# Optimization experiments

Measured on AMD Instinct MI355X. Metric: run time of the kernel, lower is better.

## Reference

```python
import jax, jax.numpy as jnp
import numpy as np

S, B, E, H, M = 1024, 4, 1024, 16, 128  # seq, batch, embed, heads, model_dims (key width)
V = E // H                              # value_dims = 64
_WSCALE = 1.0 / np.sqrt(E)              # keep softmax logits O(1)


def _cplx(re, im):
    return jax.lax.complex(re, im)


def setup_inputs() -> dict:
    key = jax.random.key(0)
    ks = jax.random.split(key, 10)
    n = lambda k, shp: jax.random.normal(k, shp, dtype=jnp.float32)
    w = lambda k, shp: n(k, shp) * np.float32(_WSCALE / np.sqrt(2.0))
    return {
        "logits_re": n(ks[0], (S, B, E)),
        "logits_im": n(ks[1], (S, B, E)),
        "wq_re": w(ks[2], (H, M, E)), "wq_im": w(ks[3], (H, M, E)),
        "wk_re": w(ks[4], (H, M, E)), "wk_im": w(ks[5], (H, M, E)),
        "wv_re": w(ks[6], (H, V, E)), "wv_im": w(ks[7], (H, V, E)),
        "wo_re": w(ks[8], (E, E)),    "wo_im": w(ks[9], (E, E)),
    }


def reference(logits_re, logits_im, wq_re, wq_im, wk_re, wk_im,
              wv_re, wv_im, wo_re, wo_im):
    x = _cplx(logits_re, logits_im)          # (s, b, e) complex64
    wq = _cplx(wq_re, wq_im)                 # (h, m, e)
    wk = _cplx(wk_re, wk_im)
    wv = _cplx(wv_re, wv_im)                 # (h, v, e)
    wo = _cplx(wo_re, wo_im)                 # (e, e)

    q = jnp.einsum('hme,sbe->bhsm', wq, x)   # (b, h, s, m)
    k = jnp.einsum('hme,sbe->bhsm', wk, x)
    v = jnp.einsum('hve,sbe->bhsv', wv, x)   # (b, h, s, v)

    scores = jnp.einsum('bhsm,bhtm->bhst', q, k)         # complex, no conjugation (matches torch matmul)
    amp = jnp.abs(scores)                                # -> float32
    causal = jnp.triu(jnp.ones((S, S), dtype=bool), 1)   # True above diagonal -> masked
    amp = jnp.where(causal, -jnp.inf, amp) / jnp.sqrt(jnp.float32(M))
    attn = jax.nn.softmax(amp, axis=-1).astype(scores.dtype)  # cast back to complex64

    upd = jnp.einsum('bhst,bhtv->bhsv', attn, v)         # (b, h, s, v)
    upd = upd.transpose(2, 0, 1, 3).reshape(S, B, E)     # 's2 b (h v)'
    out = jnp.einsum('sbe,ef->sbf', upd, wo) + x         # residual
    # complex output returned as stacked (real, imag) float32 for harness compatibility
    return jnp.stack([out.real, out.imag])
```

## Files before the change

### kernel.cpp

```cpp
#include <hip/hip_runtime.h>
#include <math.h>

#define S_DIM 1024
#define B_DIM 4
#define E_DIM 1024
#define H_DIM 16
#define M_DIM 128
#define V_DIM 64

typedef __attribute__((ext_vector_type(8))) short short8;
typedef __attribute__((ext_vector_type(4))) float f32x4;
typedef __attribute__((ext_vector_type(4))) int int4v;

__device__ __forceinline__ unsigned short f2bf(float f) {
    union { float f; unsigned u; } v; v.f = f;
    unsigned r = v.u + 0x7FFFu + ((v.u >> 16) & 1u);
    return (unsigned short)(r >> 16);
}

__device__ __forceinline__ void async16(const unsigned short* g, unsigned short* l) {
    __builtin_amdgcn_global_load_lds(
        (const __attribute__((address_space(1))) void*)g,
        (__attribute__((address_space(3))) void*)l,
        16, 0, 0);
}

__global__ __launch_bounds__(256) void convert_all(
    const float* __restrict__ xre,  const float* __restrict__ xim,
    const float* __restrict__ wqre, const float* __restrict__ wqim,
    const float* __restrict__ wkre, const float* __restrict__ wkim,
    const float* __restrict__ wvre, const float* __restrict__ wvim,
    unsigned short* __restrict__ xbre, unsigned short* __restrict__ xbim,
    unsigned short* __restrict__ wbre, unsigned short* __restrict__ wbim)
{
    const int i = blockIdx.x * 256 + threadIdx.x;
    const float *re, *im;
    unsigned short *dr, *di;
    int j;
    if (i < 1048576)      { re = xre;  im = xim;  dr = xbre;               di = xbim;               j = i; }
    else if (i < 1572864) { re = wqre; im = wqim; dr = wbre;               di = wbim;               j = i - 1048576; }
    else if (i < 2097152) { re = wkre; im = wkim; dr = wbre + 2048 * 1024; di = wbim + 2048 * 1024; j = i - 1572864; }
    else                  { re = wvre; im = wvim; dr = wbre + 4096 * 1024; di = wbim + 4096 * 1024; j = i - 2097152; }
    float4 r = ((const float4*)re)[j];
    float4 m = ((const float4*)im)[j];
    ushort4 ro, mo;
    ro.x = f2bf(r.x); ro.y = f2bf(r.y); ro.z = f2bf(r.z); ro.w = f2bf(r.w);
    mo.x = f2bf(m.x); mo.y = f2bf(m.y); mo.z = f2bf(m.z); mo.w = f2bf(m.w);
    ((ushort4*)dr)[j] = ro;
    ((ushort4*)di)[j] = mo;
}

__global__ __launch_bounds__(256) void transpose_wo(
    const float* __restrict__ wore, const float* __restrict__ woim,
    unsigned short* __restrict__ wtre, unsigned short* __restrict__ wtim)
{
    __shared__ float tr[32][33], ti[32][33];
    const int bx = blockIdx.x * 32;
    const int by = blockIdx.y * 32;
    const int tx = threadIdx.x & 31, ty = threadIdx.x >> 5;
    for (int i = ty; i < 32; i += 8) {
        tr[i][tx] = wore[(bx + i) * E_DIM + by + tx];
        ti[i][tx] = woim[(bx + i) * E_DIM + by + tx];
    }
    __syncthreads();
    for (int i = ty; i < 32; i += 8) {
        wtre[(by + i) * E_DIM + bx + tx] = f2bf(tr[tx][i]);
        wtim[(by + i) * E_DIM + bx + tx] = f2bf(ti[tx][i]);
    }
}

__global__ __launch_bounds__(256) void vtrans(
    const unsigned short* __restrict__ vrp, const unsigned short* __restrict__ vip,
    unsigned short* __restrict__ vrt, unsigned short* __restrict__ vit)
{
    __shared__ unsigned short tl[2][64][66];
    const int tid = threadIdx.x;
    const int t0 = blockIdx.x * 64;
    const int bh = blockIdx.y;
    #pragma unroll
    for (int pl = 0; pl < 2; ++pl) {
        const unsigned short* src = pl ? vip : vrp;
        #pragma unroll
        for (int p = 0; p < 2; ++p) {
            const int row = p * 32 + (tid >> 3);
            const int col = (tid & 7) * 8;
            short8 d = *(const short8*)&src[((size_t)bh * S_DIM + t0 + row) * V_DIM + col];
            #pragma unroll
            for (int j = 0; j < 8; ++j) tl[pl][row][col + j] = (unsigned short)d[j];
        }
    }
    __syncthreads();
    #pragma unroll
    for (int pl = 0; pl < 2; ++pl) {
        unsigned short* dst = pl ? vit : vrt;
        #pragma unroll
        for (int p = 0; p < 2; ++p) {
            const int v = p * 32 + (tid >> 3);
            const int tc = (tid & 7) * 8;
            short8 d;
            #pragma unroll
            for (int j = 0; j < 8; ++j) d[j] = (short)tl[pl][tc + j][v];
            *(short8*)&dst[((size_t)bh * V_DIM + v) * S_DIM + t0 + tc] = d;
        }
    }
}

template<int MODE>
__global__ __launch_bounds__(256, 2) void cgemm(
    const unsigned short* __restrict__ Are, const unsigned short* __restrict__ Aim,
    const unsigned short* __restrict__ Bre, const unsigned short* __restrict__ Bim,
    unsigned short* __restrict__ qrp, unsigned short* __restrict__ qip,
    unsigned short* __restrict__ krp, unsigned short* __restrict__ kip,
    unsigned short* __restrict__ vrp, unsigned short* __restrict__ vip,
    const float* __restrict__ xre, const float* __restrict__ xim,
    float* __restrict__ out)
{
    __shared__ __align__(16) unsigned short lds[32768];
    const int tid  = threadIdx.x;
    const int wave = tid >> 6;
    const int lane = tid & 63;
    const int r0 = blockIdx.x * 128;
    const int j0 = blockIdx.y * 128;
    const int wm = (wave >> 1) * 64;
    const int wn = (wave & 1) * 64;

    f32x4 accre[4][4], accim[4][4];
    #pragma unroll
    for (int i = 0; i < 4; ++i)
        #pragma unroll
        for (int j = 0; j < 4; ++j) {
            accre[i][j] = (f32x4){0.f, 0.f, 0.f, 0.f};
            accim[i][j] = (f32x4){0.f, 0.f, 0.f, 0.f};
        }

    const int sr   = tid >> 2;
    const int sc   = (tid & 3) * 8;
    const int scol = ((tid & 3) ^ ((tid >> 3) & 3)) * 8;

    const int fr = lane & 15;
    const int xc = ((lane >> 4) ^ ((lane >> 1) & 3)) * 8;

    #define STAGE(sl, bb) { \
        const int kg = (sl) * 32; \
        unsigned short* b_ = &lds[(bb) * 16384]; \
        const size_t ga0 = (size_t)(r0 + sr) * E_DIM + kg + scol; \
        const size_t ga1 = (size_t)(r0 + 64 + sr) * E_DIM + kg + scol; \
        const size_t gb0 = (size_t)(j0 + sr) * E_DIM + kg + scol; \
        const size_t gb1 = (size_t)(j0 + 64 + sr) * E_DIM + kg + scol; \
        async16(Are + ga0, b_ + sr * 32 + sc); \
        async16(Are + ga1, b_ + (64 + sr) * 32 + sc); \
        async16(Aim + ga0, b_ + 4096 + sr * 32 + sc); \
        async16(Aim + ga1, b_ + 4096 + (64 + sr) * 32 + sc); \
        async16(Bre + gb0, b_ + 8192 + sr * 32 + sc); \
        async16(Bre + gb1, b_ + 8192 + (64 + sr) * 32 + sc); \
        async16(Bim + gb0, b_ + 12288 + sr * 32 + sc); \
        async16(Bim + gb1, b_ + 12288 + (64 + sr) * 32 + sc); }

    STAGE(0, 0)
    asm volatile("s_waitcnt vmcnt(0)" ::: "memory");
    __builtin_amdgcn_s_barrier();

    #pragma unroll 1
    for (int s = 0; s < 32; ++s) {
        if (s < 31) STAGE(s + 1, (s + 1) & 1)

        const unsigned short* buf = &lds[(s & 1) * 16384];
        short8 ar[4], ai[4];
        #pragma unroll
        for (int im = 0; im < 4; ++im) {
            const int ro = (wm + im * 16 + fr) * 32 + xc;
            ar[im] = *(const short8*)&buf[ro];
            ai[im] = *(const short8*)&buf[4096 + ro];
        }
        #pragma unroll
        for (int jn = 0; jn < 4; ++jn) {
            const int ro = (wn + jn * 16 + fr) * 32 + xc;
            const short8 br = *(const short8*)&buf[8192 + ro];
            const short8 bi = *(const short8*)&buf[12288 + ro];
            int4v t = *(int4v*)&bi;
            t = t ^ (int)0x80008000;
            const short8 bin = *(short8*)&t;
            #pragma unroll
            for (int im = 0; im < 4; ++im) {
                accre[im][jn] = __builtin_amdgcn_mfma_f32_16x16x32_bf16(ar[im], br,  accre[im][jn], 0, 0, 0);
                accre[im][jn] = __builtin_amdgcn_mfma_f32_16x16x32_bf16(ai[im], bin, accre[im][jn], 0, 0, 0);
                accim[im][jn] = __builtin_amdgcn_mfma_f32_16x16x32_bf16(ar[im], bi,  accim[im][jn], 0, 0, 0);
                accim[im][jn] = __builtin_amdgcn_mfma_f32_16x16x32_bf16(ai[im], br,  accim[im][jn], 0, 0, 0);
            }
        }

        if (s < 31) {
            asm volatile("s_waitcnt vmcnt(0)" ::: "memory");
            __builtin_amdgcn_s_barrier();
        }
    }
    #undef STAGE

    const float qscale = 0.088388347648318447f;
    #pragma unroll
    for (int im = 0; im < 4; ++im) {
        #pragma unroll
        for (int reg = 0; reg < 4; ++reg) {
            const int r = r0 + wm + im * 16 + (lane >> 4) * 4 + reg;
            #pragma unroll
            for (int jn = 0; jn < 4; ++jn) {
                const int j = j0 + wn + jn * 16 + fr;
                const float vr = accre[im][jn][reg];
                const float vi = accim[im][jn][reg];
                if (MODE == 0) {
                    const int s = r >> 2, b = r & 3;
                    if (j < 2048) {
                        const int h = j >> 7, m = j & 127;
                        const size_t off = ((size_t)(b * H_DIM + h) * S_DIM + s) * M_DIM + m;
                        qrp[off] = f2bf(vr * qscale); qip[off] = f2bf(vi * qscale);
                    } else if (j < 4096) {
                        const int jl = j - 2048, h = jl >> 7, m = jl & 127;
                        const size_t off = ((size_t)(b * H_DIM + h) * S_DIM + s) * M_DIM + m;
                        krp[off] = f2bf(vr); kip[off] = f2bf(vi);
                    } else {
                        const int jl = j - 4096, h = jl >> 6, vv = jl & 63;
                        const size_t off = ((size_t)(b * H_DIM + h) * S_DIM + s) * V_DIM + vv;
                        vrp[off] = f2bf(vr); vip[off] = f2bf(vi);
                    }
                } else {
                    const int idx = r * E_DIM + j;
                    out[idx] = vr + xre[idx];
                    out[S_DIM * B_DIM * E_DIM + idx] = vi + xim[idx];
                }
            }
        }
    }
}

__global__ __launch_bounds__(256, 2) void attn_mfma(
    const unsigned short* __restrict__ qr, const unsigned short* __restrict__ qi,
    const unsigned short* __restrict__ kr, const unsigned short* __restrict__ ki,
    const unsigned short* __restrict__ vrt, const unsigned short* __restrict__ vit,
    unsigned short* __restrict__ updre, unsigned short* __restrict__ updim)
{
    __shared__ __align__(16) unsigned short Ks[2][64][136];
    __shared__ __align__(16) unsigned short Vs[2][64][72];
    __shared__ __align__(16) unsigned short Ps[4][16][88];

    const int tid  = threadIdx.x;
    const int wave = tid >> 6;
    const int lane = tid & 63;

    const int n  = blockIdx.x + 16 * blockIdx.y;
    const int m_ = n >> 3;
    const int bh = (n & 7) + 8 * (m_ >> 4);
    const int qt = 15 - (m_ & 15);

    const int q0 = qt * 64;
    const size_t base_qk = (size_t)bh * S_DIM * M_DIM;
    const size_t base_v  = (size_t)bh * V_DIM * S_DIM;

    const int fr = lane & 15;
    const int fg = lane >> 4;
    const int fk = fg * 8;

    const int krow = tid >> 4, kcol = (tid & 15) * 8;
    const int vrow = tid >> 3, vcol = (tid & 7) * 8;

    #pragma unroll
    for (int pl = 0; pl < 2; ++pl) {
        const unsigned short* src = pl ? qi : qr;
        #pragma unroll
        for (int p = 0; p < 4; ++p)
            *(short8*)&Ks[pl][p * 16 + krow][kcol] =
                *(const short8*)&src[base_qk + (size_t)(q0 + p * 16 + krow) * M_DIM + kcol];
    }
    __syncthreads();
    short8 Bqr[4], Bqi[4];
    {
        const int qrow = wave * 16 + fr;
        #pragma unroll
        for (int ks = 0; ks < 4; ++ks) {
            Bqr[ks] = *(const short8*)&Ks[0][qrow][ks * 32 + fk];
            Bqi[ks] = *(const short8*)&Ks[1][qrow][ks * 32 + fk];
        }
    }

    f32x4 Ore[4], Oim[4];
    #pragma unroll
    for (int vt = 0; vt < 4; ++vt) {
        Ore[vt] = (f32x4){0.f, 0.f, 0.f, 0.f};
        Oim[vt] = (f32x4){0.f, 0.f, 0.f, 0.f};
    }
    float mrun = -INFINITY, lrun = 0.f;
    const int qglob = q0 + wave * 16 + fr;

    short8 pk[2][4], pv[2][2];
    #pragma unroll
    for (int pl = 0; pl < 2; ++pl) {
        const unsigned short* src = pl ? ki : kr;
        #pragma unroll
        for (int p = 0; p < 4; ++p)
            pk[pl][p] = *(const short8*)&src[base_qk + (size_t)(p * 16 + krow) * M_DIM + kcol];
    }
    #pragma unroll
    for (int pl = 0; pl < 2; ++pl) {
        const unsigned short* src = pl ? vit : vrt;
        #pragma unroll
        for (int p = 0; p < 2; ++p)
            pv[pl][p] = *(const short8*)&src[base_v + (size_t)(p * 32 + vrow) * S_DIM + vcol];
    }

    for (int t0 = 0; t0 <= q0; t0 += 64) {
        __syncthreads();
        #pragma unroll
        for (int pl = 0; pl < 2; ++pl) {
            #pragma unroll
            for (int p = 0; p < 4; ++p)
                *(short8*)&Ks[pl][p * 16 + krow][kcol] = pk[pl][p];
            #pragma unroll
            for (int p = 0; p < 2; ++p)
                *(short8*)&Vs[pl][p * 32 + vrow][vcol] = pv[pl][p];
        }
        __syncthreads();

        if (t0 + 64 <= q0) {
            const int tn = t0 + 64;
            #pragma unroll
            for (int pl = 0; pl < 2; ++pl) {
                const unsigned short* src = pl ? ki : kr;
                #pragma unroll
                for (int p = 0; p < 4; ++p)
                    pk[pl][p] = *(const short8*)&src[base_qk + (size_t)(tn + p * 16 + krow) * M_DIM + kcol];
            }
            #pragma unroll
            for (int pl = 0; pl < 2; ++pl) {
                const unsigned short* src = pl ? vit : vrt;
                #pragma unroll
                for (int p = 0; p < 2; ++p)
                    pv[pl][p] = *(const short8*)&src[base_v + (size_t)(p * 32 + vrow) * S_DIM + tn + vcol];
            }
        }

        f32x4 Sre[4], Sim[4];
        __builtin_amdgcn_s_setprio(1);
        #pragma unroll
        for (int tt = 0; tt < 4; ++tt) {
            Sre[tt] = (f32x4){0.f, 0.f, 0.f, 0.f};
            Sim[tt] = (f32x4){0.f, 0.f, 0.f, 0.f};
            const int trow = tt * 16 + fr;
            #pragma unroll
            for (int ks = 0; ks < 4; ++ks) {
                const short8 Akr = *(const short8*)&Ks[0][trow][ks * 32 + fk];
                const short8 Aki = *(const short8*)&Ks[1][trow][ks * 32 + fk];
                int4v t = *(int4v*)&Aki;
                t = t ^ (int)0x80008000;
                const short8 Akin = *(short8*)&t;
                Sre[tt] = __builtin_amdgcn_mfma_f32_16x16x32_bf16(Akr,  Bqr[ks], Sre[tt], 0, 0, 0);
                Sre[tt] = __builtin_amdgcn_mfma_f32_16x16x32_bf16(Akin, Bqi[ks], Sre[tt], 0, 0, 0);
                Sim[tt] = __builtin_amdgcn_mfma_f32_16x16x32_bf16(Akr,  Bqi[ks], Sim[tt], 0, 0, 0);
                Sim[tt] = __builtin_amdgcn_mfma_f32_16x16x32_bf16(Aki,  Bqr[ks], Sim[tt], 0, 0, 0);
            }
        }
        __builtin_amdgcn_s_setprio(0);

        float rowmax = -INFINITY;
        #pragma unroll
        for (int tt = 0; tt < 4; ++tt) {
            #pragma unroll
            for (int r = 0; r < 4; ++r) {
                const int tg = t0 + tt * 16 + fg * 4 + r;
                const float re = Sre[tt][r], im = Sim[tt][r];
                const float a = sqrtf(re * re + im * im);
                const float av = (tg > qglob) ? -INFINITY : a;
                Sre[tt][r] = av;
                rowmax = fmaxf(rowmax, av);
            }
        }
        rowmax = fmaxf(rowmax, __shfl_xor(rowmax, 16));
        rowmax = fmaxf(rowmax, __shfl_xor(rowmax, 32));

        if (!__all(rowmax - mrun <= 8.0f)) {
            const float nm = fmaxf(mrun, rowmax);
            const float alpha = __expf(mrun - nm);
            mrun = nm;
            lrun *= alpha;
            #pragma unroll
            for (int vt = 0; vt < 4; ++vt)
                #pragma unroll
                for (int r = 0; r < 4; ++r) { Ore[vt][r] *= alpha; Oim[vt][r] *= alpha; }
        }

        float psum = 0.f;
        #pragma unroll
        for (int tt = 0; tt < 4; ++tt) {
            const float p0 = __expf(Sre[tt][0] - mrun);
            const float p1 = __expf(Sre[tt][1] - mrun);
            const float p2 = __expf(Sre[tt][2] - mrun);
            const float p3 = __expf(Sre[tt][3] - mrun);
            psum += p0 + p1 + p2 + p3;
            ushort4 pw;
            pw.x = f2bf(p0); pw.y = f2bf(p1); pw.z = f2bf(p2); pw.w = f2bf(p3);
            *(ushort4*)&Ps[wave][fr][tt * 16 + fg * 4] = pw;
        }
        psum += __shfl_xor(psum, 16);
        psum += __shfl_xor(psum, 32);
        lrun += psum;

        const short8 Bp0 = *(const short8*)&Ps[wave][fr][fk];
        const short8 Bp1 = *(const short8*)&Ps[wave][fr][32 + fk];
        __builtin_amdgcn_s_setprio(1);
        #pragma unroll
        for (int vt = 0; vt < 4; ++vt) {
            const int vr2 = vt * 16 + fr;
            const short8 Ar0 = *(const short8*)&Vs[0][vr2][fk];
            const short8 Ar1 = *(const short8*)&Vs[0][vr2][32 + fk];
            const short8 Ai0 = *(const short8*)&Vs[1][vr2][fk];
            const short8 Ai1 = *(const short8*)&Vs[1][vr2][32 + fk];
            Ore[vt] = __builtin_amdgcn_mfma_f32_16x16x32_bf16(Ar0, Bp0, Ore[vt], 0, 0, 0);
            Ore[vt] = __builtin_amdgcn_mfma_f32_16x16x32_bf16(Ar1, Bp1, Ore[vt], 0, 0, 0);
            Oim[vt] = __builtin_amdgcn_mfma_f32_16x16x32_bf16(Ai0, Bp0, Oim[vt], 0, 0, 0);
            Oim[vt] = __builtin_amdgcn_mfma_f32_16x16x32_bf16(Ai1, Bp1, Oim[vt], 0, 0, 0);
        }
        __builtin_amdgcn_s_setprio(0);
    }

    const int b = bh >> 4, h = bh & 15;
    const float inv = 1.0f / lrun;
    const size_t base = ((size_t)(qglob * B_DIM + b)) * E_DIM + h * V_DIM;
    #pragma unroll
    for (int vt = 0; vt < 4; ++vt) {
        ushort4 pr, pi;
        pr.x = f2bf(Ore[vt][0] * inv); pr.y = f2bf(Ore[vt][1] * inv);
        pr.z = f2bf(Ore[vt][2] * inv); pr.w = f2bf(Ore[vt][3] * inv);
        pi.x = f2bf(Oim[vt][0] * inv); pi.y = f2bf(Oim[vt][1] * inv);
        pi.z = f2bf(Oim[vt][2] * inv); pi.w = f2bf(Oim[vt][3] * inv);
        *(ushort4*)&updre[base + vt * 16 + fg * 4] = pr;
        *(ushort4*)&updim[base + vt * 16 + fg * 4] = pi;
    }
}

extern "C" void kernel_launch(void* const* d_in, const int* in_sizes, int n_in,
                              void* d_out, int out_size, void* d_ws, size_t ws_size,
                              hipStream_t stream) {
    const float* xre  = (const float*)d_in[0];
    const float* xim  = (const float*)d_in[1];
    const float* wqre = (const float*)d_in[2];
    const float* wqim = (const float*)d_in[3];
    const float* wkre = (const float*)d_in[4];
    const float* wkim = (const float*)d_in[5];
    const float* wvre = (const float*)d_in[6];
    const float* wvim = (const float*)d_in[7];
    const float* wore = (const float*)d_in[8];
    const float* woim = (const float*)d_in[9];
    float* out = (float*)d_out;

    char* p = (char*)d_ws;
    const size_t QK = (size_t)B_DIM * H_DIM * S_DIM * M_DIM;
    const size_t VS = (size_t)B_DIM * H_DIM * S_DIM * V_DIM;
    const size_t SBE = (size_t)S_DIM * B_DIM * E_DIM;
    unsigned short* qrw = (unsigned short*)p;  p += QK * 2;
    unsigned short* qiw = (unsigned short*)p;  p += QK * 2;
    unsigned short* krw = (unsigned short*)p;  p += QK * 2;
    unsigned short* kiw = (unsigned short*)p;  p += QK * 2;
    unsigned short* vrw = (unsigned short*)p;  p += VS * 2;
    unsigned short* viw = (unsigned short*)p;  p += VS * 2;
    unsigned short* vrt = (unsigned short*)p;  p += VS * 2;
    unsigned short* vit = (unsigned short*)p;  p += VS * 2;
    unsigned short* updre = (unsigned short*)p; p += SBE * 2;
    unsigned short* updim = (unsigned short*)p; p += SBE * 2;
    unsigned short* xbre  = (unsigned short*)p; p += SBE * 2;
    unsigned short* xbim  = (unsigned short*)p; p += SBE * 2;
    unsigned short* wbre  = (unsigned short*)p; p += (size_t)5120 * E_DIM * 2;
    unsigned short* wbim  = (unsigned short*)p; p += (size_t)5120 * E_DIM * 2;
    unsigned short* wtre  = (unsigned short*)p; p += (size_t)E_DIM * E_DIM * 2;
    unsigned short* wtim  = (unsigned short*)p; p += (size_t)E_DIM * E_DIM * 2;

    convert_all<<<9216, 256, 0, stream>>>(xre, xim, wqre, wqim, wkre, wkim, wvre, wvim,
                                          xbre, xbim, wbre, wbim);
    transpose_wo<<<dim3(32, 32), 256, 0, stream>>>(wore, woim, wtre, wtim);

    cgemm<0><<<dim3(32, 40), 256, 0, stream>>>(xbre, xbim, wbre, wbim,
                                               qrw, qiw, krw, kiw, vrw, viw,
                                               nullptr, nullptr, nullptr);
    vtrans<<<dim3(16, 64), 256, 0, stream>>>(vrw, viw, vrt, vit);
    attn_mfma<<<dim3(16, 64), 256, 0, stream>>>(qrw, qiw, krw, kiw, vrt, vit, updre, updim);
    cgemm<1><<<dim3(32, 8), 256, 0, stream>>>(updre, updim, wtre, wtim,
                                              nullptr, nullptr, nullptr, nullptr, nullptr, nullptr,
                                              xre, xim, out);
}
```

Measured before the change: 449.9 us.

## Enlarge attention query tile to 128 rows and halve output-GEMM row tile

The attention kernel now runs 512 threads (8 waves) per block covering 128 query rows. Each K/V tile is staged once into LDS and shared by twice as many waves, and Q fragments are loaded straight from global memory. Waves in the lower half skip tiles beyond their causal limit while still taking part in staging. The output-projection GEMM switches to 64-row tiles with a 3-block occupancy hint so the grid has twice as many blocks to fill the CUs, at the cost of less reuse of the B tile.

```diff
diff --git a/kernel.cpp b/kernel.cpp
--- a/kernel.cpp
+++ b/kernel.cpp
@@ -106,7 +106,7 @@
 }
 
 template<int MODE>
-__global__ __launch_bounds__(256, 2) void cgemm(
+__global__ __launch_bounds__(256, MODE ? 3 : 2) void cgemm(
     const unsigned short* __restrict__ Are, const unsigned short* __restrict__ Aim,
     const unsigned short* __restrict__ Bre, const unsigned short* __restrict__ Bim,
     unsigned short* __restrict__ qrp, unsigned short* __restrict__ qip,
@@ -115,18 +115,22 @@
     const float* __restrict__ xre, const float* __restrict__ xim,
     float* __restrict__ out)
 {
-    __shared__ __align__(16) unsigned short lds[32768];
+    constexpr int BM  = MODE ? 64 : 128;
+    constexpr int IM  = MODE ? 2 : 4;
+    constexpr int ASZ = BM * 32;
+    constexpr int BUF = 2 * ASZ + 8192;
+    __shared__ __align__(16) unsigned short lds[2 * BUF];
     const int tid  = threadIdx.x;
     const int wave = tid >> 6;
     const int lane = tid & 63;
-    const int r0 = blockIdx.x * 128;
+    const int r0 = blockIdx.x * BM;
     const int j0 = blockIdx.y * 128;
-    const int wm = (wave >> 1) * 64;
+    const int wm = (wave >> 1) * (MODE ? 32 : 64);
     const int wn = (wave & 1) * 64;
 
-    f32x4 accre[4][4], accim[4][4];
-    #pragma unroll
-    for (int i = 0; i < 4; ++i)
+    f32x4 accre[IM][4], accim[IM][4];
+    #pragma unroll
+    for (int i = 0; i < IM; ++i)
         #pragma unroll
         for (int j = 0; j < 4; ++j) {
             accre[i][j] = (f32x4){0.f, 0.f, 0.f, 0.f};
@@ -142,19 +146,21 @@
 
     #define STAGE(sl, bb) { \
         const int kg = (sl) * 32; \
-        unsigned short* b_ = &lds[(bb) * 16384]; \
+        unsigned short* b_ = &lds[(bb) * BUF]; \
         const size_t ga0 = (size_t)(r0 + sr) * E_DIM + kg + scol; \
-        const size_t ga1 = (size_t)(r0 + 64 + sr) * E_DIM + kg + scol; \
         const size_t gb0 = (size_t)(j0 + sr) * E_DIM + kg + scol; \
         const size_t gb1 = (size_t)(j0 + 64 + sr) * E_DIM + kg + scol; \
         async16(Are + ga0, b_ + sr * 32 + sc); \
-        async16(Are + ga1, b_ + (64 + sr) * 32 + sc); \
-        async16(Aim + ga0, b_ + 4096 + sr * 32 + sc); \
-        async16(Aim + ga1, b_ + 4096 + (64 + sr) * 32 + sc); \
-        async16(Bre + gb0, b_ + 8192 + sr * 32 + sc); \
-        async16(Bre + gb1, b_ + 8192 + (64 + sr) * 32 + sc); \
-        async16(Bim + gb0, b_ + 12288 + sr * 32 + sc); \
-        async16(Bim + gb1, b_ + 12288 + (64 + sr) * 32 + sc); }
+        async16(Aim + ga0, b_ + ASZ + sr * 32 + sc); \
+        if (MODE == 0) { \
+            const size_t ga1 = (size_t)(r0 + 64 + sr) * E_DIM + kg + scol; \
+            async16(Are + ga1, b_ + (64 + sr) * 32 + sc); \
+            async16(Aim + ga1, b_ + ASZ + (64 + sr) * 32 + sc); \
+        } \
+        async16(Bre + gb0, b_ + 2 * ASZ + sr * 32 + sc); \
+        async16(Bre + gb1, b_ + 2 * ASZ + (64 + sr) * 32 + sc); \
+        async16(Bim + gb0, b_ + 2 * ASZ + 4096 + sr * 32 + sc); \
+        async16(Bim + gb1, b_ + 2 * ASZ + 4096 + (64 + sr) * 32 + sc); }
 
     STAGE(0, 0)
     asm volatile("s_waitcnt vmcnt(0)" ::: "memory");
@@ -164,24 +170,24 @@
     for (int s = 0; s < 32; ++s) {
         if (s < 31) STAGE(s + 1, (s + 1) & 1)
 
-        const unsigned short* buf = &lds[(s & 1) * 16384];
-        short8 ar[4], ai[4];
-        #pragma unroll
-        for (int im = 0; im < 4; ++im) {
+        const unsigned short* buf = &lds[(s & 1) * BUF];
+        short8 ar[IM], ai[IM];
+        #pragma unroll
+        for (int im = 0; im < IM; ++im) {
             const int ro = (wm + im * 16 + fr) * 32 + xc;
             ar[im] = *(const short8*)&buf[ro];
-            ai[im] = *(const short8*)&buf[4096 + ro];
+            ai[im] = *(const short8*)&buf[ASZ + ro];
         }
         #pragma unroll
         for (int jn = 0; jn < 4; ++jn) {
             const int ro = (wn + jn * 16 + fr) * 32 + xc;
-            const short8 br = *(const short8*)&buf[8192 + ro];
-            const short8 bi = *(const short8*)&buf[12288 + ro];
+            const short8 br = *(const short8*)&buf[2 * ASZ + ro];
+            const short8 bi = *(const short8*)&buf[2 * ASZ + 4096 + ro];
             int4v t = *(int4v*)&bi;
             t = t ^ (int)0x80008000;
             const short8 bin = *(short8*)&t;
             #pragma unroll
-            for (int im = 0; im < 4; ++im) {
+            for (int im = 0; im < IM; ++im) {
                 accre[im][jn] = __builtin_amdgcn_mfma_f32_16x16x32_bf16(ar[im], br,  accre[im][jn], 0, 0, 0);
                 accre[im][jn] = __builtin_amdgcn_mfma_f32_16x16x32_bf16(ai[im], bin, accre[im][jn], 0, 0, 0);
                 accim[im][jn] = __builtin_amdgcn_mfma_f32_16x16x32_bf16(ar[im], bi,  accim[im][jn], 0, 0, 0);
@@ -198,7 +204,7 @@
 
     const float qscale = 0.088388347648318447f;
     #pragma unroll
-    for (int im = 0; im < 4; ++im) {
+    for (int im = 0; im < IM; ++im) {
         #pragma unroll
         for (int reg = 0; reg < 4; ++reg) {
             const int r = r0 + wm + im * 16 + (lane >> 4) * 4 + reg;
@@ -232,7 +238,7 @@
     }
 }
 
-__global__ __launch_bounds__(256, 2) void attn_mfma(
+__global__ __launch_bounds__(512, 4) void attn_mfma(
     const unsigned short* __restrict__ qr, const unsigned short* __restrict__ qi,
     const unsigned short* __restrict__ kr, const unsigned short* __restrict__ ki,
     const unsigned short* __restrict__ vrt, const unsigned short* __restrict__ vit,
@@ -240,18 +246,17 @@
 {
     __shared__ __align__(16) unsigned short Ks[2][64][136];
     __shared__ __align__(16) unsigned short Vs[2][64][72];
-    __shared__ __align__(16) unsigned short Ps[4][16][88];
+    __shared__ __align__(16) unsigned short Ps[8][16][88];
 
     const int tid  = threadIdx.x;
     const int wave = tid >> 6;
     const int lane = tid & 63;
 
-    const int n  = blockIdx.x + 16 * blockIdx.y;
-    const int m_ = n >> 3;
-    const int bh = (n & 7) + 8 * (m_ >> 4);
-    const int qt = 15 - (m_ & 15);
-
-    const int q0 = qt * 64;
+    const int n  = blockIdx.x + 8 * blockIdx.y;
+    const int bh = (n & 7) + 8 * (n >> 6);
+    const int qt = 7 - ((n >> 3) & 7);
+
+    const int q0 = qt * 128;
     const size_t base_qk = (size_t)bh * S_DIM * M_DIM;
     const size_t base_v  = (size_t)bh * V_DIM * S_DIM;
 
@@ -262,22 +267,13 @@
     const int krow = tid >> 4, kcol = (tid & 15) * 8;
     const int vrow = tid >> 3, vcol = (tid & 7) * 8;
 
-    #pragma unroll
-    for (int pl = 0; pl < 2; ++pl) {
-        const unsigned short* src = pl ? qi : qr;
-        #pragma unroll
-        for (int p = 0; p < 4; ++p)
-            *(short8*)&Ks[pl][p * 16 + krow][kcol] =
-                *(const short8*)&src[base_qk + (size_t)(q0 + p * 16 + krow) * M_DIM + kcol];
-    }
-    __syncthreads();
     short8 Bqr[4], Bqi[4];
     {
-        const int qrow = wave * 16 + fr;
+        const size_t qo = base_qk + (size_t)(q0 + wave * 16 + fr) * M_DIM + fk;
         #pragma unroll
         for (int ks = 0; ks < 4; ++ks) {
-            Bqr[ks] = *(const short8*)&Ks[0][qrow][ks * 32 + fk];
-            Bqi[ks] = *(const short8*)&Ks[1][qrow][ks * 32 + fk];
+            Bqr[ks] = *(const short8*)&qr[qo + ks * 32];
+            Bqi[ks] = *(const short8*)&qi[qo + ks * 32];
         }
     }
 
@@ -289,53 +285,50 @@
     }
     float mrun = -INFINITY, lrun = 0.f;
     const int qglob = q0 + wave * 16 + fr;
-
-    short8 pk[2][4], pv[2][2];
+    const int qcap  = q0 + (wave >> 2) * 64;
+
+    short8 pk[2][2], pv[2];
     #pragma unroll
     for (int pl = 0; pl < 2; ++pl) {
         const unsigned short* src = pl ? ki : kr;
         #pragma unroll
-        for (int p = 0; p < 4; ++p)
-            pk[pl][p] = *(const short8*)&src[base_qk + (size_t)(p * 16 + krow) * M_DIM + kcol];
+        for (int p = 0; p < 2; ++p)
+            pk[pl][p] = *(const short8*)&src[base_qk + (size_t)(p * 32 + krow) * M_DIM + kcol];
     }
     #pragma unroll
     for (int pl = 0; pl < 2; ++pl) {
         const unsigned short* src = pl ? vit : vrt;
-        #pragma unroll
-        for (int p = 0; p < 2; ++p)
-            pv[pl][p] = *(const short8*)&src[base_v + (size_t)(p * 32 + vrow) * S_DIM + vcol];
-    }
-
-    for (int t0 = 0; t0 <= q0; t0 += 64) {
+        pv[pl] = *(const short8*)&src[base_v + (size_t)vrow * S_DIM + vcol];
+    }
+
+    for (int t0 = 0; t0 <= q0 + 64; t0 += 64) {
         __syncthreads();
         #pragma unroll
         for (int pl = 0; pl < 2; ++pl) {
             #pragma unroll
-            for (int p = 0; p < 4; ++p)
-                *(short8*)&Ks[pl][p * 16 + krow][kcol] = pk[pl][p];
-            #pragma unroll
             for (int p = 0; p < 2; ++p)
-                *(short8*)&Vs[pl][p * 32 + vrow][vcol] = pv[pl][p];
+                *(short8*)&Ks[pl][p * 32 + krow][kcol] = pk[pl][p];
+            *(short8*)&Vs[pl][vrow][vcol] = pv[pl];
         }
         __syncthreads();
 
-        if (t0 + 64 <= q0) {
+        if (t0 <= q0) {
             const int tn = t0 + 64;
             #pragma unroll
             for (int pl = 0; pl < 2; ++pl) {
                 const unsigned short* src = pl ? ki : kr;
                 #pragma unroll
-                for (int p = 0; p < 4; ++p)
-                    pk[pl][p] = *(const short8*)&src[base_qk + (size_t)(tn + p * 16 + krow) * M_DIM + kcol];
+                for (int p = 0; p < 2; ++p)
+                    pk[pl][p] = *(const short8*)&src[base_qk + (size_t)(tn + p * 32 + krow) * M_DIM + kcol];
             }
             #pragma unroll
             for (int pl = 0; pl < 2; ++pl) {
                 const unsigned short* src = pl ? vit : vrt;
-                #pragma unroll
-                for (int p = 0; p < 2; ++p)
-                    pv[pl][p] = *(const short8*)&src[base_v + (size_t)(p * 32 + vrow) * S_DIM + tn + vcol];
-            }
-        }
+                pv[pl] = *(const short8*)&src[base_v + (size_t)vrow * S_DIM + tn + vcol];
+            }
+        }
+
+        if (t0 > qcap) continue;
 
         f32x4 Sre[4], Sim[4];
         __builtin_amdgcn_s_setprio(1);
@@ -479,8 +472,8 @@
                                                qrw, qiw, krw, kiw, vrw, viw,
                                                nullptr, nullptr, nullptr);
     vtrans<<<dim3(16, 64), 256, 0, stream>>>(vrw, viw, vrt, vit);
-    attn_mfma<<<dim3(16, 64), 256, 0, stream>>>(qrw, qiw, krw, kiw, vrt, vit, updre, updim);
-    cgemm<1><<<dim3(32, 8), 256, 0, stream>>>(updre, updim, wtre, wtim,
+    attn_mfma<<<dim3(8, 64), 512, 0, stream>>>(qrw, qiw, krw, kiw, vrt, vit, updre, updim);
+    cgemm<1><<<dim3(64, 8), 256, 0, stream>>>(updre, updim, wtre, wtim,
                                               nullptr, nullptr, nullptr, nullptr, nullptr, nullptr,
                                               xre, xim, out);
 }
```

After: 484.7 us. +7.7%, slower.
